# Performance work log

Measured on AMD Instinct MI355X. Metric: run time of the kernel, lower is better.

The kernel has to match this reference:

```python
import jax, jax.numpy as jnp
import numpy as np

DIM = 768; DEPTH = 8; HEADS = 12; DH = 64; DFF = 2048
SOFTCLAMP = 50.0; TIME_EVERY = 4
B, T, S = 2, 32, 256
EPS = 1e-6


def rmsnorm(x, w):
    return x * jax.lax.rsqrt(jnp.mean(x * x, axis=-1, keepdims=True) + EPS) * w


def l2norm(x):
    n = jnp.sqrt(jnp.sum(x * x, axis=-1, keepdims=True))
    return x / jnp.maximum(n, 1e-12)


def make_rotary(n):
    inv = 1.0 / (10000.0 ** (jnp.arange(0, DH, 2, dtype=jnp.float32) / DH))
    f = jnp.arange(n, dtype=jnp.float32)[:, None] * inv[None, :]
    return jnp.concatenate([f, f], axis=-1)  # (n, DH)


def apply_rot(rot, x):
    # x: (B', H, n, DH), rot: (n, DH)
    x1, x2 = jnp.split(x, 2, axis=-1)
    return x * jnp.cos(rot) + jnp.concatenate([-x2, x1], axis=-1) * jnp.sin(rot)


def attn_block(x, rv, nw, wq, wk, wv, wo, wg, wmix, bm, kgam, rot, causal):
    # x: (B', n, DIM); rv: (B', H, n, DH) value-residual
    Bp, n, _ = x.shape
    tn = rmsnorm(x, nw)
    q = (tn @ wq).reshape(Bp, n, HEADS, DH).transpose(0, 2, 1, 3)
    k = (tn @ wk).reshape(Bp, n, HEADS, DH).transpose(0, 2, 1, 3)
    v = (tn @ wv).reshape(Bp, n, HEADS, DH).transpose(0, 2, 1, 3)
    # learned value-residual lerp: v <- v + mix * (rv - v)
    mix = jax.nn.sigmoid(tn @ wmix + bm).transpose(0, 2, 1)[..., None]
    v = v + mix * (rv - v)
    # MultiHeadRMSNorm on keys: l2norm * (gamma+1) * sqrt(DH)
    k = l2norm(k) * ((kgam + 1.0) * (DH ** 0.5))[:, None, :]
    if rot is not None:
        q = apply_rot(rot, q)
        k = apply_rot(rot, k)
    sim = jnp.einsum('bhid,bhjd->bhij', q, k) * (DH ** -0.5)
    sim = jnp.tanh(sim / SOFTCLAMP) * SOFTCLAMP
    if causal:
        cm = jnp.triu(jnp.ones((n, n), dtype=bool), 1)
        sim = jnp.where(cm, -jnp.finfo(sim.dtype).max, sim)
    attn = jax.nn.softmax(sim, axis=-1)
    o = jnp.einsum('bhij,bhjd->bhid', attn, v)
    gates = jax.nn.sigmoid(tn @ wg).transpose(0, 2, 1)[..., None]
    o = o * gates
    o = o.transpose(0, 2, 1, 3).reshape(Bp, n, HEADS * DH)
    return o @ wo


def ff_block(x, nw, win, bi, wout, bo):
    tn = rmsnorm(x, nw)
    h = tn @ win + bi
    a, g = jnp.split(h, 2, axis=-1)
    return (a * jax.nn.gelu(g, approximate=False)) @ wout + bo


def setup_inputs() -> dict:
    key = jax.random.key(0)
    ks = jax.random.split(key, 16)
    def rn(k, shape, scale=0.02):
        return jax.random.normal(k, shape, dtype=jnp.float32) * scale
    return {
        'tokens': jax.random.normal(ks[0], (B, T, S, DIM), dtype=jnp.float32),
        'attn_norm_w': jnp.ones((DEPTH, DIM), jnp.float32),
        'Wq': rn(ks[1], (DEPTH, DIM, HEADS * DH)),
        'Wk': rn(ks[2], (DEPTH, DIM, HEADS * DH)),
        'Wv': rn(ks[3], (DEPTH, DIM, HEADS * DH)),
        'Wo': rn(ks[4], (DEPTH, HEADS * DH, DIM)),
        'Wg': rn(ks[5], (DEPTH, DIM, HEADS)),
        'Wmix': rn(ks[6], (DEPTH, DIM, HEADS)),
        'bmix': jnp.zeros((DEPTH, HEADS), jnp.float32),
        'k_gamma': rn(ks[7], (DEPTH, HEADS, DH)),
        'ff_norm_w': jnp.ones((DEPTH, DIM), jnp.float32),
        'Win': rn(ks[8], (DEPTH, DIM, 2 * DFF)),
        'b_in': jnp.zeros((DEPTH, 2 * DFF), jnp.float32),
        'Wout': rn(ks[9], (DEPTH, DFF, DIM)),
        'b_out': jnp.zeros((DEPTH, DIM), jnp.float32),
        'vr_norm_w': jnp.ones((DIM,), jnp.float32),
        'vr_W': rn(ks[10], (DIM, HEADS * DH)),
        'final_norm_w': jnp.ones((DIM,), jnp.float32),
    }


def reference(tokens, attn_norm_w, Wq, Wk, Wv, Wo, Wg, Wmix, bmix, k_gamma,
              ff_norm_w, Win, b_in, Wout, b_out, vr_norm_w, vr_W, final_norm_w):
    b, t, s, d = tokens.shape
    # value residuals computed once from the input tokens
    rv = (rmsnorm(tokens, vr_norm_w) @ vr_W).reshape(b, t, s, HEADS, DH)
    rot = make_rotary(t)
    x = tokens
    for i in range(DEPTH):
        is_time = ((i + 1) % TIME_EVERY == 0)
        if is_time:
            xa = x.transpose(0, 2, 1, 3).reshape(b * s, t, d)
            rva = rv.transpose(0, 2, 3, 1, 4).reshape(b * s, HEADS, t, DH)
            o = attn_block(xa, rva, attn_norm_w[i], Wq[i], Wk[i], Wv[i], Wo[i],
                           Wg[i], Wmix[i], bmix[i], k_gamma[i], rot, True)
            o = o.reshape(b, s, t, d).transpose(0, 2, 1, 3)
        else:
            xa = x.reshape(b * t, s, d)
            rva = rv.transpose(0, 1, 3, 2, 4).reshape(b * t, HEADS, s, DH)
            o = attn_block(xa, rva, attn_norm_w[i], Wq[i], Wk[i], Wv[i], Wo[i],
                           Wg[i], Wmix[i], bmix[i], k_gamma[i], None, False)
            o = o.reshape(b, t, s, d)
        x = x + o
        x = x + ff_block(x, ff_norm_w[i], Win[i], b_in[i], Wout[i], b_out[i])
    return rmsnorm(x, final_norm_w)
```

## Files before the change

kernel.cpp:

```cpp
#include <hip/hip_runtime.h>
#include <cmath>

#define DIM 768
#define DEPTH 8
#define HEADS 12
#define DH 64
#define DFF 2048
#define NTOK 16384
#define BB 2
#define TT 32
#define SS 256
#define LDQ 2304

typedef __attribute__((ext_vector_type(8))) short short8;
typedef __attribute__((ext_vector_type(4))) float f32x4;

__device__ __forceinline__ float sigmoidf_(float x) { return 1.0f / (1.0f + __expf(-x)); }
__device__ __forceinline__ float geluf_(float x) {
  float z = fabsf(x) * 0.70710678118654752f;
  float t = __builtin_amdgcn_rcpf(fmaf(0.3275911f, z, 1.0f));
  float poly = t * fmaf(t, fmaf(t, fmaf(t, fmaf(t, 1.061405429f, -1.453152027f),
                    1.421413741f), -0.284496736f), 0.254829592f);
  float erfv = 1.0f - poly * __expf(-z * z);
  erfv = copysignf(erfv, x);
  return 0.5f * x * (1.0f + erfv);
}
__device__ __forceinline__ unsigned short f2bf(float x) {
  union { float f; unsigned int u; } a; a.f = x;
  unsigned int r = a.u + 0x7fff + ((a.u >> 16) & 1);
  return (unsigned short)(r >> 16);
}
__device__ __forceinline__ float bf2f(unsigned short h) {
  union { unsigned int u; float f; } a; a.u = ((unsigned int)h) << 16;
  return a.f;
}
__device__ __forceinline__ void load_lds16(const void* g, void* l) {
  __builtin_amdgcn_global_load_lds(
      (const __attribute__((address_space(1))) unsigned int*)g,
      (__attribute__((address_space(3))) unsigned int*)l, 16, 0, 0);
}
__device__ __forceinline__ float softclamp_exp(float sv) {
  float a = exp2f(sv * 0.057707802f);
  float rc = __builtin_amdgcn_rcpf(a + 1.0f);
  return exp2f(fmaf(-144.26950408f, rc, 72.13475204f));
}

template<int BF>
__global__ __launch_bounds__(256) void rmsnorm_kernel(
    const float* __restrict__ x, const float* __restrict__ w, void* __restrict__ outp)
{
  int row = blockIdx.x;
  int tid = threadIdx.x;
  const float* xr = x + (size_t)row * DIM;
  float v0 = xr[tid], v1 = xr[tid + 256], v2 = xr[tid + 512];
  float ss = v0 * v0 + v1 * v1 + v2 * v2;
  #pragma unroll
  for (int off = 32; off; off >>= 1) ss += __shfl_xor(ss, off);
  __shared__ float sred[4];
  if ((tid & 63) == 0) sred[tid >> 6] = ss;
  __syncthreads();
  float tot = sred[0] + sred[1] + sred[2] + sred[3];
  float r = rsqrtf(tot * (1.0f / DIM) + 1e-6f);
  if (BF) {
    unsigned short* orow = (unsigned short*)outp + (size_t)row * DIM;
    orow[tid]       = f2bf(v0 * r * w[tid]);
    orow[tid + 256] = f2bf(v1 * r * w[tid + 256]);
    orow[tid + 512] = f2bf(v2 * r * w[tid + 512]);
  } else {
    float* orow = (float*)outp + (size_t)row * DIM;
    orow[tid]       = v0 * r * w[tid];
    orow[tid + 256] = v1 * r * w[tid + 256];
    orow[tid + 512] = v2 * r * w[tid + 512];
  }
}

__global__ __launch_bounds__(256) void w_to_bt(
    const float* __restrict__ W, unsigned short* __restrict__ WT, int K, int N)
{
  __shared__ float t[32][33];
  int n0 = blockIdx.x * 32, k0 = blockIdx.y * 32;
  int c = threadIdx.x & 31, r8 = threadIdx.x >> 5;
  #pragma unroll
  for (int rr = r8; rr < 32; rr += 8)
    t[rr][c] = W[(size_t)(k0 + rr) * N + n0 + c];
  __syncthreads();
  #pragma unroll
  for (int rn = r8; rn < 32; rn += 8)
    WT[(size_t)(n0 + rn) * K + k0 + c] = f2bf(t[c][rn]);
}

__global__ __launch_bounds__(256) void w_convert_layer(
    const float* __restrict__ Wq, const float* __restrict__ Wk,
    const float* __restrict__ Wv, const float* __restrict__ Wo,
    const float* __restrict__ Win, const float* __restrict__ Wout,
    unsigned short* __restrict__ wqkvT, unsigned short* __restrict__ woT,
    unsigned short* __restrict__ winT, unsigned short* __restrict__ woutT)
{
  __shared__ float tle[32][33];
  int t = blockIdx.x;
  const float* W; unsigned short* WT; int K, N, n0, k0, glu = 0;
  if (t < 1728) {
    int rg = t / 576, tt = t - rg * 576;
    W = (rg == 0) ? Wq : (rg == 1) ? Wk : Wv;
    WT = wqkvT + (size_t)rg * 768 * 768;
    K = 768; N = 768; n0 = (tt % 24) * 32; k0 = (tt / 24) * 32;
  } else if (t < 2304) {
    int tt = t - 1728; W = Wo; WT = woT;
    K = 768; N = 768; n0 = (tt % 24) * 32; k0 = (tt / 24) * 32;
  } else if (t < 5376) {
    int tt = t - 2304; W = Win; WT = winT;
    K = 768; N = 4096; n0 = (tt % 128) * 32; k0 = (tt / 128) * 32; glu = 1;
  } else {
    int tt = t - 5376; W = Wout; WT = woutT;
    K = 2048; N = 768; n0 = (tt % 24) * 32; k0 = (tt / 24) * 32;
  }
  int c = threadIdx.x & 31, r8 = threadIdx.x >> 5;
  int col = n0 + c;
  int scol = col;
  if (glu) {
    int b = col >> 5, rr2 = col & 31;
    scol = (rr2 < 16) ? (b * 16 + rr2) : (2048 + b * 16 + rr2 - 16);
  }
  for (int rr = r8; rr < 32; rr += 8)
    tle[rr][c] = W[(size_t)(k0 + rr) * N + scol];
  __syncthreads();
  for (int rn = r8; rn < 32; rn += 8)
    WT[(size_t)(n0 + rn) * K + k0 + c] = f2bf(tle[c][rn]);
}

template<int MODE>
__global__ __launch_bounds__(256) void gemm_bf16(
    const unsigned short* __restrict__ A, const unsigned short* __restrict__ BT,
    float* __restrict__ Cf, unsigned short* __restrict__ Hg,
    const float* __restrict__ bias, int M, int N, int K)
{
  __shared__ unsigned short As[128 * 64];
  __shared__ unsigned short Bs[128 * 64];
  const int tid = threadIdx.x;
  const int wave = tid >> 6;
  const int lane = tid & 63;
  const int bm = blockIdx.y * 128;
  const int bn = blockIdx.x * 128;
  const int wm = (wave & 1) * 64;
  const int wn = (wave >> 1) * 64;

  f32x4 acc[4][4];
  #pragma unroll
  for (int i = 0; i < 4; ++i)
    #pragma unroll
    for (int j = 0; j < 4; ++j) acc[i][j] = (f32x4){0.f, 0.f, 0.f, 0.f};

  const int srow = wave * 8 + (lane >> 3);
  const int sku = ((lane & 7) ^ (lane >> 3)) * 8;
  const unsigned short* gA = A + (size_t)(bm + srow) * K + sku;
  const unsigned short* gB = BT + (size_t)(bn + srow) * K + sku;
  unsigned short* lA = &As[wave * 512];
  unsigned short* lB = &Bs[wave * 512];

  const int fr = lane & 15;
  const int fg = lane >> 4;

  for (int k0 = 0; k0 < K; k0 += 64) {
    #pragma unroll
    for (int it = 0; it < 4; ++it) {
      load_lds16(gA + k0 + (size_t)(it * 32) * K, lA + it * 2048);
      load_lds16(gB + k0 + (size_t)(it * 32) * K, lB + it * 2048);
    }
    __syncthreads();
    #pragma unroll
    for (int s = 0; s < 2; ++s) {
      short8 a[4], b[4];
      #pragma unroll
      for (int i = 0; i < 4; ++i) {
        int row = wm + 16 * i + fr;
        a[i] = *(const short8*)&As[row * 64 + (((s * 4 + fg) ^ (row & 7)) << 3)];
      }
      #pragma unroll
      for (int j = 0; j < 4; ++j) {
        int row = wn + 16 * j + fr;
        b[j] = *(const short8*)&Bs[row * 64 + (((s * 4 + fg) ^ (row & 7)) << 3)];
      }
      #pragma unroll
      for (int i = 0; i < 4; ++i)
        #pragma unroll
        for (int j = 0; j < 4; ++j)
          acc[i][j] = __builtin_amdgcn_mfma_f32_16x16x32_bf16(a[i], b[j], acc[i][j], 0, 0, 0);
    }
    __syncthreads();
  }

  const int crow0 = bm + wm + (lane >> 4) * 4;
  const int ccol0 = bn + wn + fr;
  float bv[4];
  if (MODE != 3) {
    #pragma unroll
    for (int j = 0; j < 4; ++j) bv[j] = bias ? bias[ccol0 + 16 * j] : 0.0f;
  }
  #pragma unroll
  for (int i = 0; i < 4; ++i) {
    #pragma unroll
    for (int r = 0; r < 4; ++r) {
      int row = crow0 + 16 * i + r;
      if (MODE == 3) {
        #pragma unroll
        for (int pj = 0; pj < 2; ++pj) {
          int b32 = (bn + wn + 32 * pj) >> 5;
          float av = acc[i][2 * pj][r] + bias[b32 * 16 + fr];
          float gv = acc[i][2 * pj + 1][r] + bias[2048 + b32 * 16 + fr];
          Hg[(size_t)row * (N >> 1) + b32 * 16 + fr] = f2bf(av * geluf_(gv));
        }
      } else {
        #pragma unroll
        for (int j = 0; j < 4; ++j) {
          int col = ccol0 + 16 * j;
          size_t idx = (size_t)row * N + col;
          float val = acc[i][j][r] + bv[j];
          if (MODE == 0) Cf[idx] = val;
          else if (MODE == 1) Cf[idx] += val;
          else Hg[idx] = f2bf(val);
        }
      }
    }
  }
}

__global__ __launch_bounds__(256) void proj12x2_kernel(
    const unsigned short* __restrict__ A, const float* __restrict__ Bw1,
    const float* __restrict__ b1, const float* __restrict__ Bw2,
    float* __restrict__ out1, float* __restrict__ out2)
{
  int row = blockIdx.x * 4 + (threadIdx.x >> 6);
  int lane = threadIdx.x & 63;
  const unsigned short* ar = A + (size_t)row * DIM;
  float acc1[HEADS], acc2[HEADS];
  #pragma unroll
  for (int j = 0; j < HEADS; ++j) { acc1[j] = 0.0f; acc2[j] = 0.0f; }
  for (int k2 = lane; k2 < DIM; k2 += 64) {
    float a = bf2f(ar[k2]);
    const float* bw1 = Bw1 + (size_t)k2 * HEADS;
    const float* bw2 = Bw2 + (size_t)k2 * HEADS;
    #pragma unroll
    for (int j = 0; j < HEADS; ++j) {
      acc1[j] = fmaf(a, bw1[j], acc1[j]);
      acc2[j] = fmaf(a, bw2[j], acc2[j]);
    }
  }
  #pragma unroll
  for (int j = 0; j < HEADS; ++j) {
    #pragma unroll
    for (int off = 32; off; off >>= 1) {
      acc1[j] += __shfl_xor(acc1[j], off);
      acc2[j] += __shfl_xor(acc2[j], off);
    }
  }
  if (lane < HEADS) {
    out1[(size_t)row * HEADS + lane] = sigmoidf_(acc1[lane] + b1[lane]);
    out2[(size_t)row * HEADS + lane] = sigmoidf_(acc2[lane]);
  }
}

__global__ __launch_bounds__(768) void qkv_fix_kernel(
    unsigned short* __restrict__ qkv, const unsigned short* __restrict__ rvb,
    const float* __restrict__ mix, const float* __restrict__ kgam, int is_time)
{
  int tok = blockIdx.x;
  int h = threadIdx.x >> 6;
  int d = threadIdx.x & 63;
  size_t rowb = (size_t)tok * LDQ + h * DH + d;
  float kv = bf2f(qkv[rowb + 768]);
  float ss = kv * kv;
  #pragma unroll
  for (int off = 32; off; off >>= 1) ss += __shfl_xor(ss, off);
  float nrm = fmaxf(sqrtf(ss), 1e-12f);
  kv = kv / nrm * (kgam[h * DH + d] + 1.0f) * 8.0f;
  float mv = mix[(size_t)tok * HEADS + h];
  float vv = bf2f(qkv[rowb + 1536]);
  float rvv = bf2f(rvb[(size_t)tok * DIM + h * DH + d]);
  qkv[rowb + 1536] = f2bf(vv + mv * (rvv - vv));
  float qv = bf2f(qkv[rowb]);
  if (is_time) {
    int t = (tok >> 8) & 31;
    int j = d & 31;
    float ang = (float)t * __expf(-(float)j * (9.210340371976184f / 32.0f));
    float cs = cosf(ang), sn = sinf(ang);
    float qp = __shfl_xor(qv, 32);
    float kp = __shfl_xor(kv, 32);
    float sgn = (d < 32) ? -1.0f : 1.0f;
    qv = qv * cs + sgn * qp * sn;
    kv = kv * cs + sgn * kp * sn;
  }
  qkv[rowb] = f2bf(qv);
  qkv[rowb + 768] = f2bf(kv);
}

__global__ __launch_bounds__(256, 2) void attn_mfma_kernel(
    const unsigned short* __restrict__ q, const unsigned short* __restrict__ k,
    const unsigned short* __restrict__ v, const unsigned short* __restrict__ rvb,
    const float* __restrict__ mix, const float* __restrict__ gate,
    const float* __restrict__ kgam, unsigned short* __restrict__ o)
{
  __shared__ __align__(16) unsigned short Ks[128 * 64];
  __shared__ __align__(16) unsigned short VsT[64 * 128];
  __shared__ __align__(16) unsigned short Pw[4][32 * 64];
  const int tid = threadIdx.x;
  const int wave = tid >> 6;
  const int lane = tid & 63;
  const int g = lane >> 4;
  const int c16 = lane & 15;
  const int bp = blockIdx.x >> 1;
  const int qh = blockIdx.x & 1;
  const int h = blockIdx.y;
  const size_t qoff = (size_t)bp * SS * LDQ + h * DH;
  const int qbase = qh * 128 + wave * 32;

  short8 aq[2][2];
  #pragma unroll
  for (int i = 0; i < 2; ++i) {
    const unsigned short* qp = q + qoff + (size_t)(qbase + i * 16 + c16) * LDQ;
    #pragma unroll
    for (int cc = 0; cc < 2; ++cc)
      aq[i][cc] = *(const short8*)(qp + cc * 32 + g * 8);
  }

  f32x4 oacc[2][4];
  float rs[2][4];
  #pragma unroll
  for (int i = 0; i < 2; ++i)
    #pragma unroll
    for (int j = 0; j < 4; ++j) {
      oacc[i][j] = (f32x4){0.f, 0.f, 0.f, 0.f};
      rs[i][j] = 0.f;
    }

  for (int half = 0; half < 2; ++half) {
    const int r0 = half * 128;
    #pragma unroll
    for (int it = 0; it < 4; ++it) {
      int f = tid + it * 256;
      int row = f >> 3, u = f & 7;
      short8 t8 = *(const short8*)(k + qoff + (size_t)(r0 + row) * LDQ + u * 8);
      float kv[8];
      float ss = 0.f;
      #pragma unroll
      for (int c = 0; c < 8; ++c) { kv[c] = bf2f((unsigned short)t8[c]); ss += kv[c] * kv[c]; }
      ss += __shfl_xor(ss, 1); ss += __shfl_xor(ss, 2); ss += __shfl_xor(ss, 4);
      float inv = 8.0f / fmaxf(sqrtf(ss), 1e-12f);
      float4 kg0 = *(const float4*)(kgam + h * DH + u * 8);
      float4 kg1 = *(const float4*)(kgam + h * DH + u * 8 + 4);
      short8 o8;
      o8[0] = (short)f2bf(kv[0] * inv * (kg0.x + 1.0f));
      o8[1] = (short)f2bf(kv[1] * inv * (kg0.y + 1.0f));
      o8[2] = (short)f2bf(kv[2] * inv * (kg0.z + 1.0f));
      o8[3] = (short)f2bf(kv[3] * inv * (kg0.w + 1.0f));
      o8[4] = (short)f2bf(kv[4] * inv * (kg1.x + 1.0f));
      o8[5] = (short)f2bf(kv[5] * inv * (kg1.y + 1.0f));
      o8[6] = (short)f2bf(kv[6] * inv * (kg1.z + 1.0f));
      o8[7] = (short)f2bf(kv[7] * inv * (kg1.w + 1.0f));
      *(short8*)&Ks[row * 64 + ((u ^ (row & 7)) << 3)] = o8;
    }
    #pragma unroll
    for (int it = 0; it < 4; ++it) {
      int f = tid + it * 256;
      int j = f & 127, dq = f >> 7;
      int tok = bp * SS + r0 + j;
      short8 v8 = *(const short8*)(v + qoff + (size_t)(r0 + j) * LDQ + dq * 8);
      short8 r8 = *(const short8*)(rvb + (size_t)tok * DIM + h * DH + dq * 8);
      float mv = mix[(size_t)tok * HEADS + h];
      int u = j >> 3;
      #pragma unroll
      for (int c = 0; c < 8; ++c) {
        int d = dq * 8 + c;
        float vv = bf2f((unsigned short)v8[c]);
        float val = vv + mv * (bf2f((unsigned short)r8[c]) - vv);
        VsT[d * 128 + ((u ^ (d & 15)) << 3) + (j & 7)] = f2bf(val);
      }
    }
    __syncthreads();

    #pragma unroll
    for (int jc = 0; jc < 2; ++jc) {
      const int lr0 = jc * 64;
      #pragma unroll
      for (int jh = 0; jh < 2; ++jh) {
        f32x4 s[2][2];
        #pragma unroll
        for (int i = 0; i < 2; ++i)
          #pragma unroll
          for (int j = 0; j < 2; ++j) s[i][j] = (f32x4){0.f, 0.f, 0.f, 0.f};
        #pragma unroll
        for (int j2 = 0; j2 < 2; ++j2) {
          int jt = jh * 2 + j2;
          int row = lr0 + jt * 16 + c16;
          short8 b0 = *(const short8*)&Ks[row * 64 + ((g ^ (row & 7)) << 3)];
          short8 b1 = *(const short8*)&Ks[row * 64 + (((4 + g) ^ (row & 7)) << 3)];
          #pragma unroll
          for (int i = 0; i < 2; ++i) {
            s[i][j2] = __builtin_amdgcn_mfma_f32_16x16x32_bf16(aq[i][0], b0, s[i][j2], 0, 0, 0);
            s[i][j2] = __builtin_amdgcn_mfma_f32_16x16x32_bf16(aq[i][1], b1, s[i][j2], 0, 0, 0);
          }
        }
        #pragma unroll
        for (int i = 0; i < 2; ++i) {
          #pragma unroll
          for (int j2 = 0; j2 < 2; ++j2) {
            int pj = (jh * 2 + j2) * 16 + c16;
            int uj = pj >> 3;
            #pragma unroll
            for (int r = 0; r < 4; ++r) {
              float p = softclamp_exp(s[i][j2][r] * 0.125f);
              unsigned short pb = f2bf(p);
              rs[i][r] += bf2f(pb);
              int prow = i * 16 + g * 4 + r;
              Pw[wave][prow * 64 + ((uj ^ (prow & 7)) << 3) + (pj & 7)] = pb;
            }
          }
        }
      }
      #pragma unroll
      for (int jj = 0; jj < 2; ++jj) {
        short8 pa[2];
        #pragma unroll
        for (int i = 0; i < 2; ++i) {
          int prow = i * 16 + c16;
          int u = jj * 4 + g;
          pa[i] = *(const short8*)&Pw[wave][prow * 64 + ((u ^ (prow & 7)) << 3)];
        }
        const int jl = lr0 + jj * 32 + g * 8;
        const int uv = jl >> 3;
        #pragma unroll
        for (int dt = 0; dt < 4; ++dt) {
          int d = dt * 16 + c16;
          short8 bv = *(const short8*)&VsT[d * 128 + ((uv ^ (d & 15)) << 3)];
          #pragma unroll
          for (int i = 0; i < 2; ++i)
            oacc[i][dt] = __builtin_amdgcn_mfma_f32_16x16x32_bf16(pa[i], bv, oacc[i][dt], 0, 0, 0);
        }
      }
    }
    __syncthreads();
  }

  #pragma unroll
  for (int i = 0; i < 2; ++i)
    #pragma unroll
    for (int r = 0; r < 4; ++r) {
      float t = rs[i][r];
      t += __shfl_xor(t, 1); t += __shfl_xor(t, 2);
      t += __shfl_xor(t, 4); t += __shfl_xor(t, 8);
      rs[i][r] = t;
    }
  #pragma unroll
  for (int i = 0; i < 2; ++i) {
    #pragma unroll
    for (int r = 0; r < 4; ++r) {
      int row = qbase + i * 16 + g * 4 + r;
      int tq = bp * SS + row;
      float gt = gate[(size_t)tq * HEADS + h] / rs[i][r];
      unsigned short* op = o + (size_t)tq * DIM + h * DH;
      #pragma unroll
      for (int dt = 0; dt < 4; ++dt)
        op[dt * 16 + c16] = f2bf(oacc[i][dt][r] * gt);
    }
  }
}

__global__ __launch_bounds__(256, 2) void attn_time_mfma(
    const unsigned short* __restrict__ q, const unsigned short* __restrict__ k,
    const unsigned short* __restrict__ v, const float* __restrict__ gate,
    unsigned short* __restrict__ o)
{
  __shared__ __align__(16) unsigned short VT[4][64 * 32];
  __shared__ __align__(16) unsigned short Pw[4][32 * 32];
  const int tid = threadIdx.x;
  const int wave = tid >> 6;
  const int lane = tid & 63;
  const int g = lane >> 4;
  const int c16 = lane & 15;
  const int h = blockIdx.y;
  const int sp = blockIdx.x * 4 + wave;
  const int base = (sp >> 8) * (TT * SS) + (sp & 255);

  short8 aq[2][2], bk[2][2];
  #pragma unroll
  for (int i = 0; i < 2; ++i) {
    const unsigned short* qp = q + (size_t)(base + (i * 16 + c16) * SS) * LDQ + h * DH;
    const unsigned short* kp = k + (size_t)(base + (i * 16 + c16) * SS) * LDQ + h * DH;
    #pragma unroll
    for (int cc = 0; cc < 2; ++cc) {
      aq[i][cc] = *(const short8*)(qp + cc * 32 + g * 8);
      bk[i][cc] = *(const short8*)(kp + cc * 32 + g * 8);
    }
  }

  {
    int tp = lane >> 1;
    int dh0 = (lane & 1) * 32;
    const unsigned short* vp = v + (size_t)(base + tp * SS) * LDQ + h * DH + dh0;
    int ut = tp >> 3;
    #pragma unroll
    for (int j4 = 0; j4 < 4; ++j4) {
      short8 t = *(const short8*)(vp + j4 * 8);
      #pragma unroll
      for (int c = 0; c < 8; ++c) {
        int d = dh0 + j4 * 8 + c;
        VT[wave][d * 32 + ((ut ^ (d & 3)) << 3) + (tp & 7)] = (unsigned short)t[c];
      }
    }
  }

  f32x4 s[2][2];
  #pragma unroll
  for (int i = 0; i < 2; ++i)
    #pragma unroll
    for (int j = 0; j < 2; ++j) s[i][j] = (f32x4){0.f, 0.f, 0.f, 0.f};
  #pragma unroll
  for (int jt = 0; jt < 2; ++jt)
    #pragma unroll
    for (int i = 0; i < 2; ++i) {
      s[i][jt] = __builtin_amdgcn_mfma_f32_16x16x32_bf16(aq[i][0], bk[jt][0], s[i][jt], 0, 0, 0);
      s[i][jt] = __builtin_amdgcn_mfma_f32_16x16x32_bf16(aq[i][1], bk[jt][1], s[i][jt], 0, 0, 0);
    }

  float rs[2][4];
  #pragma unroll
  for (int i = 0; i < 2; ++i)
    #pragma unroll
    for (int r = 0; r < 4; ++r) rs[i][r] = 0.f;
  #pragma unroll
  for (int i = 0; i < 2; ++i) {
    #pragma unroll
    for (int jt = 0; jt < 2; ++jt) {
      int pj = jt * 16 + c16;
      int uj = pj >> 3;
      #pragma unroll
      for (int r = 0; r < 4; ++r) {
        int t = i * 16 + g * 4 + r;
        float p = softclamp_exp(s[i][jt][r] * 0.125f);
        unsigned short pb = (pj <= t) ? f2bf(p) : (unsigned short)0;
        rs[i][r] += bf2f(pb);
        Pw[wave][t * 32 + ((uj ^ (t & 3)) << 3) + (pj & 7)] = pb;
      }
    }
  }

  short8 pa[2];
  #pragma unroll
  for (int i = 0; i < 2; ++i) {
    int prow = i * 16 + c16;
    pa[i] = *(const short8*)&Pw[wave][prow * 32 + ((g ^ (prow & 3)) << 3)];
  }
  f32x4 oacc[2][4];
  #pragma unroll
  for (int dt = 0; dt < 4; ++dt) {
    int d = dt * 16 + c16;
    short8 bv = *(const short8*)&VT[wave][d * 32 + ((g ^ (d & 3)) << 3)];
    #pragma unroll
    for (int i = 0; i < 2; ++i)
      oacc[i][dt] = __builtin_amdgcn_mfma_f32_16x16x32_bf16(
          pa[i], bv, (f32x4){0.f, 0.f, 0.f, 0.f}, 0, 0, 0);
  }

  #pragma unroll
  for (int i = 0; i < 2; ++i)
    #pragma unroll
    for (int r = 0; r < 4; ++r) {
      float t = rs[i][r];
      t += __shfl_xor(t, 1); t += __shfl_xor(t, 2);
      t += __shfl_xor(t, 4); t += __shfl_xor(t, 8);
      rs[i][r] = t;
    }
  #pragma unroll
  for (int i = 0; i < 2; ++i) {
    #pragma unroll
    for (int r = 0; r < 4; ++r) {
      int t = i * 16 + g * 4 + r;
      int tok = base + t * SS;
      float gt = gate[(size_t)tok * HEADS + h] / rs[i][r];
      unsigned short* op = o + (size_t)tok * DIM + h * DH;
      #pragma unroll
      for (int dt = 0; dt < 4; ++dt)
        op[dt * 16 + c16] = f2bf(oacc[i][dt][r] * gt);
    }
  }
}

extern "C" void kernel_launch(void* const* d_in, const int* in_sizes, int n_in,
                              void* d_out, int out_size, void* d_ws, size_t ws_size,
                              hipStream_t stream)
{
  const float* tokens = (const float*)d_in[0];
  const float* attn_norm_w = (const float*)d_in[1];
  const float* Wq   = (const float*)d_in[2];
  const float* Wk   = (const float*)d_in[3];
  const float* Wv   = (const float*)d_in[4];
  const float* Wo   = (const float*)d_in[5];
  const float* Wg   = (const float*)d_in[6];
  const float* Wmix = (const float*)d_in[7];
  const float* bmix = (const float*)d_in[8];
  const float* kgam = (const float*)d_in[9];
  const float* ffw  = (const float*)d_in[10];
  const float* Win  = (const float*)d_in[11];
  const float* bin  = (const float*)d_in[12];
  const float* Wout = (const float*)d_in[13];
  const float* bout = (const float*)d_in[14];
  const float* vrw  = (const float*)d_in[15];
  const float* vrW  = (const float*)d_in[16];
  const float* fnw  = (const float*)d_in[17];

  const size_t NT = (size_t)NTOK * DIM;
  float* ws  = (float*)d_ws;
  float* x   = ws;
  float* mix = x + NT;
  float* gate = mix + (size_t)NTOK * HEADS;
  unsigned short* tn   = (unsigned short*)(gate + (size_t)NTOK * HEADS);
  unsigned short* qkv  = tn + NT;
  unsigned short* rvb  = qkv + (size_t)NTOK * LDQ;
  unsigned short* wqkvT = rvb + NT;
  unsigned short* woT  = wqkvT + (size_t)2304 * 768;
  unsigned short* winT = woT + (size_t)768 * 768;
  unsigned short* woutT= winT + (size_t)4096 * 768;
  unsigned short* vrWT = woutT + (size_t)768 * 2048;
  unsigned short* hg   = qkv;

  hipMemcpyAsync(x, tokens, NT * sizeof(float), hipMemcpyDeviceToDevice, stream);

  w_to_bt<<<dim3(24, 24), 256, 0, stream>>>(vrW, vrWT, DIM, DIM);
  rmsnorm_kernel<1><<<NTOK, 256, 0, stream>>>(tokens, vrw, tn);
  gemm_bf16<2><<<dim3(6, 128), 256, 0, stream>>>(
      tn, vrWT, nullptr, rvb, nullptr, NTOK, DIM, DIM);

  for (int i = 0; i < DEPTH; ++i) {
    int is_time = ((i + 1) % 4 == 0) ? 1 : 0;
    w_convert_layer<<<6912, 256, 0, stream>>>(
        Wq + (size_t)i * DIM * DIM, Wk + (size_t)i * DIM * DIM,
        Wv + (size_t)i * DIM * DIM, Wo + (size_t)i * DIM * DIM,
        Win + (size_t)i * DIM * 2 * DFF, Wout + (size_t)i * DFF * DIM,
        wqkvT, woT, winT, woutT);

    rmsnorm_kernel<1><<<NTOK, 256, 0, stream>>>(x, attn_norm_w + (size_t)i * DIM, tn);
    gemm_bf16<2><<<dim3(18, 128), 256, 0, stream>>>(
        tn, wqkvT, nullptr, qkv, nullptr, NTOK, LDQ, DIM);
    proj12x2_kernel<<<NTOK / 4, 256, 0, stream>>>(
        tn, Wmix + (size_t)i * DIM * HEADS, bmix + (size_t)i * HEADS,
        Wg + (size_t)i * DIM * HEADS, mix, gate);
    if (is_time) {
      qkv_fix_kernel<<<dim3(NTOK), 768, 0, stream>>>(
          qkv, rvb, mix, kgam + (size_t)i * HEADS * DH, is_time);
      attn_time_mfma<<<dim3((BB * SS) / 4, HEADS), 256, 0, stream>>>(
          qkv, qkv + 768, qkv + 1536, gate, tn);
    } else {
      attn_mfma_kernel<<<dim3(BB * TT * 2, HEADS), 256, 0, stream>>>(
          qkv, qkv + 768, qkv + 1536, rvb, mix, gate,
          kgam + (size_t)i * HEADS * DH, tn);
    }
    gemm_bf16<1><<<dim3(6, 128), 256, 0, stream>>>(tn, woT, x, nullptr, nullptr, NTOK, DIM, DIM);
    rmsnorm_kernel<1><<<NTOK, 256, 0, stream>>>(x, ffw + (size_t)i * DIM, tn);
    gemm_bf16<3><<<dim3(32, 128), 256, 0, stream>>>(
        tn, winT, nullptr, hg, bin + (size_t)i * 2 * DFF, NTOK, 2 * DFF, DIM);
    gemm_bf16<1><<<dim3(6, 128), 256, 0, stream>>>(
        hg, woutT, x, nullptr, bout + (size_t)i * DIM, NTOK, DIM, DFF);
  }
  rmsnorm_kernel<0><<<NTOK, 256, 0, stream>>>(x, fnw, (float*)d_out);
}
```

Measured before the change: 4.429 ms.

## Rewrite bf16 GEMM as 256x256 tile with double-buffered LDS ping-pong pipeline

```diff
diff --git a/kernel.cpp b/kernel.cpp
--- a/kernel.cpp
+++ b/kernel.cpp
@@ -129,67 +129,122 @@
 }
 
 template<int MODE>
-__global__ __launch_bounds__(256) void gemm_bf16(
+__global__ __launch_bounds__(512, 2) void gemm_bf16(
     const unsigned short* __restrict__ A, const unsigned short* __restrict__ BT,
     float* __restrict__ Cf, unsigned short* __restrict__ Hg,
     const float* __restrict__ bias, int M, int N, int K)
 {
-  __shared__ unsigned short As[128 * 64];
-  __shared__ unsigned short Bs[128 * 64];
+  __shared__ unsigned short As[2][256 * 64];
+  __shared__ unsigned short Bs[2][256 * 64];
   const int tid = threadIdx.x;
   const int wave = tid >> 6;
   const int lane = tid & 63;
-  const int bm = blockIdx.y * 128;
-  const int bn = blockIdx.x * 128;
-  const int wm = (wave & 1) * 64;
-  const int wn = (wave >> 1) * 64;
-
-  f32x4 acc[4][4];
-  #pragma unroll
-  for (int i = 0; i < 4; ++i)
-    #pragma unroll
-    for (int j = 0; j < 4; ++j) acc[i][j] = (f32x4){0.f, 0.f, 0.f, 0.f};
-
-  const int srow = wave * 8 + (lane >> 3);
-  const int sku = ((lane & 7) ^ (lane >> 3)) * 8;
-  const unsigned short* gA = A + (size_t)(bm + srow) * K + sku;
-  const unsigned short* gB = BT + (size_t)(bn + srow) * K + sku;
-  unsigned short* lA = &As[wave * 512];
-  unsigned short* lB = &Bs[wave * 512];
-
+  const int bm = blockIdx.y * 256;
+  const int bn = blockIdx.x * 256;
+  const int wm = (wave >> 2) * 128;
+  const int wn = (wave & 3) * 64;
   const int fr = lane & 15;
   const int fg = lane >> 4;
 
-  for (int k0 = 0; k0 < K; k0 += 64) {
-    #pragma unroll
-    for (int it = 0; it < 4; ++it) {
-      load_lds16(gA + k0 + (size_t)(it * 32) * K, lA + it * 2048);
-      load_lds16(gB + k0 + (size_t)(it * 32) * K, lB + it * 2048);
-    }
-    __syncthreads();
-    #pragma unroll
-    for (int s = 0; s < 2; ++s) {
-      short8 a[4], b[4];
-      #pragma unroll
-      for (int i = 0; i < 4; ++i) {
-        int row = wm + 16 * i + fr;
-        a[i] = *(const short8*)&As[row * 64 + (((s * 4 + fg) ^ (row & 7)) << 3)];
-      }
-      #pragma unroll
-      for (int j = 0; j < 4; ++j) {
-        int row = wn + 16 * j + fr;
-        b[j] = *(const short8*)&Bs[row * 64 + (((s * 4 + fg) ^ (row & 7)) << 3)];
-      }
-      #pragma unroll
-      for (int i = 0; i < 4; ++i)
-        #pragma unroll
-        for (int j = 0; j < 4; ++j)
-          acc[i][j] = __builtin_amdgcn_mfma_f32_16x16x32_bf16(a[i], b[j], acc[i][j], 0, 0, 0);
-    }
-    __syncthreads();
-  }
-
-  const int crow0 = bm + wm + (lane >> 4) * 4;
+  f32x4 acc[8][4];
+  #pragma unroll
+  for (int i = 0; i < 8; ++i)
+    #pragma unroll
+    for (int j = 0; j < 4; ++j) acc[i][j] = (f32x4){0.f, 0.f, 0.f, 0.f};
+
+  const unsigned short* gA0 = A + (size_t)(bm + wave * 8 + (lane >> 3)) * K
+                                + (((lane & 7) ^ (lane >> 3)) << 3);
+  const unsigned short* gB0 = BT + (size_t)(bn + wave * 8 + (lane >> 3)) * K
+                                 + (((lane & 7) ^ (lane >> 3)) << 3);
+
+#define STAGE_A(KT_, H_) { \
+  load_lds16(gA0 + (size_t)(128 * (H_)) * K + (KT_) * 64, \
+             &As[(KT_) & 1][(128 * (H_) + wave * 8) * 64]); \
+  load_lds16(gA0 + (size_t)(128 * (H_) + 64) * K + (KT_) * 64, \
+             &As[(KT_) & 1][(128 * (H_) + 64 + wave * 8) * 64]); }
+#define STAGE_B(KT_, H_) { \
+  load_lds16(gB0 + (size_t)(128 * (H_)) * K + (KT_) * 64, \
+             &Bs[(KT_) & 1][(128 * (H_) + wave * 8) * 64]); \
+  load_lds16(gB0 + (size_t)(128 * (H_) + 64) * K + (KT_) * 64, \
+             &Bs[(KT_) & 1][(128 * (H_) + 64 + wave * 8) * 64]); }
+
+  short8 a[4][2], b[2][2];
+
+#define LDA_HALF(IB, SL) { \
+  _Pragma("unroll") for (int ii = 0; ii < 4; ++ii) { \
+    int row_ = wm + 16 * ((IB) + ii) + fr; \
+    int rx_ = (row_ & 7) << 3; \
+    a[ii][0] = *(const short8*)&As[SL][row_ * 64 + ((fg << 3) ^ rx_)]; \
+    a[ii][1] = *(const short8*)&As[SL][row_ * 64 + ((32 + (fg << 3)) ^ rx_)]; } }
+#define LDB_PAIR(JB, SL) { \
+  _Pragma("unroll") for (int jj = 0; jj < 2; ++jj) { \
+    int row_ = wn + 16 * ((JB) + jj) + fr; \
+    int rx_ = (row_ & 7) << 3; \
+    b[jj][0] = *(const short8*)&Bs[SL][row_ * 64 + ((fg << 3) ^ rx_)]; \
+    b[jj][1] = *(const short8*)&Bs[SL][row_ * 64 + ((32 + (fg << 3)) ^ rx_)]; } }
+#define MFMA_Q(IB, JB) { \
+  _Pragma("unroll") for (int ii = 0; ii < 4; ++ii) \
+  _Pragma("unroll") for (int jj = 0; jj < 2; ++jj) { \
+    acc[(IB)+ii][(JB)+jj] = __builtin_amdgcn_mfma_f32_16x16x32_bf16( \
+        a[ii][0], b[jj][0], acc[(IB)+ii][(JB)+jj], 0, 0, 0); \
+    acc[(IB)+ii][(JB)+jj] = __builtin_amdgcn_mfma_f32_16x16x32_bf16( \
+        a[ii][1], b[jj][1], acc[(IB)+ii][(JB)+jj], 0, 0, 0); } }
+#define PH_MID() \
+  __builtin_amdgcn_s_barrier(); \
+  asm volatile("s_waitcnt lgkmcnt(0)" ::: "memory"); \
+  __builtin_amdgcn_sched_barrier(0); \
+  __builtin_amdgcn_s_setprio(1);
+#define PH_END() \
+  __builtin_amdgcn_s_setprio(0); \
+  __builtin_amdgcn_s_barrier();
+
+  const int KT = K >> 6;
+  const int ITERS = KT >> 1;
+
+  STAGE_A(0, 0); STAGE_A(0, 1); STAGE_B(0, 0); STAGE_B(0, 1); STAGE_A(1, 0);
+  asm volatile("s_waitcnt vmcnt(2)" ::: "memory");
+  __builtin_amdgcn_s_barrier();
+
+  for (int it = 0; it < ITERS; ++it) {
+    const int c1 = 2 * it + 1;
+    const int n0 = 2 * it + 2;
+    const bool last = (it == ITERS - 1);
+    LDA_HALF(0, 0); LDB_PAIR(0, 0);
+    STAGE_A(c1, 1);
+    PH_MID(); MFMA_Q(0, 0); PH_END();
+    LDB_PAIR(2, 0);
+    STAGE_B(c1, 0);
+    PH_MID(); MFMA_Q(0, 2); PH_END();
+    LDA_HALF(4, 0); LDB_PAIR(0, 0);
+    STAGE_B(c1, 1);
+    PH_MID(); MFMA_Q(4, 0); PH_END();
+    LDB_PAIR(2, 0);
+    if (n0 < KT) STAGE_A(n0, 0);
+    PH_MID(); MFMA_Q(4, 2);
+    __builtin_amdgcn_s_setprio(0);
+    if (!last) asm volatile("s_waitcnt vmcnt(2)" ::: "memory");
+    else       asm volatile("s_waitcnt vmcnt(0)" ::: "memory");
+    __builtin_amdgcn_s_barrier();
+    LDA_HALF(0, 1); LDB_PAIR(0, 1);
+    if (n0 < KT) STAGE_A(n0, 1);
+    PH_MID(); MFMA_Q(0, 0); PH_END();
+    LDB_PAIR(2, 1);
+    if (n0 < KT) STAGE_B(n0, 0);
+    PH_MID(); MFMA_Q(0, 2); PH_END();
+    LDA_HALF(4, 1); LDB_PAIR(0, 1);
+    if (n0 < KT) STAGE_B(n0, 1);
+    PH_MID(); MFMA_Q(4, 0); PH_END();
+    LDB_PAIR(2, 1);
+    if (c1 + 2 < KT) STAGE_A(c1 + 2, 0);
+    PH_MID(); MFMA_Q(4, 2);
+    __builtin_amdgcn_s_setprio(0);
+    if (!last) {
+      asm volatile("s_waitcnt vmcnt(2)" ::: "memory");
+      __builtin_amdgcn_s_barrier();
+    }
+  }
+
+  const int crow0 = bm + wm + ((lane >> 4) << 2);
   const int ccol0 = bn + wn + fr;
   float bv[4];
   if (MODE != 3) {
@@ -197,7 +252,7 @@
     for (int j = 0; j < 4; ++j) bv[j] = bias ? bias[ccol0 + 16 * j] : 0.0f;
   }
   #pragma unroll
-  for (int i = 0; i < 4; ++i) {
+  for (int i = 0; i < 8; ++i) {
     #pragma unroll
     for (int r = 0; r < 4; ++r) {
       int row = crow0 + 16 * i + r;
@@ -222,6 +277,13 @@
       }
     }
   }
+#undef STAGE_A
+#undef STAGE_B
+#undef LDA_HALF
+#undef LDB_PAIR
+#undef MFMA_Q
+#undef PH_MID
+#undef PH_END
 }
 
 __global__ __launch_bounds__(256) void proj12x2_kernel(
@@ -626,7 +688,7 @@
 
   w_to_bt<<<dim3(24, 24), 256, 0, stream>>>(vrW, vrWT, DIM, DIM);
   rmsnorm_kernel<1><<<NTOK, 256, 0, stream>>>(tokens, vrw, tn);
-  gemm_bf16<2><<<dim3(6, 128), 256, 0, stream>>>(
+  gemm_bf16<2><<<dim3(3, 64), 512, 0, stream>>>(
       tn, vrWT, nullptr, rvb, nullptr, NTOK, DIM, DIM);
 
   for (int i = 0; i < DEPTH; ++i) {
@@ -638,7 +700,7 @@
         wqkvT, woT, winT, woutT);
 
     rmsnorm_kernel<1><<<NTOK, 256, 0, stream>>>(x, attn_norm_w + (size_t)i * DIM, tn);
-    gemm_bf16<2><<<dim3(18, 128), 256, 0, stream>>>(
+    gemm_bf16<2><<<dim3(9, 64), 512, 0, stream>>>(
         tn, wqkvT, nullptr, qkv, nullptr, NTOK, LDQ, DIM);
     proj12x2_kernel<<<NTOK / 4, 256, 0, stream>>>(
         tn, Wmix + (size_t)i * DIM * HEADS, bmix + (size_t)i * HEADS,
@@ -653,11 +715,11 @@
           qkv, qkv + 768, qkv + 1536, rvb, mix, gate,
           kgam + (size_t)i * HEADS * DH, tn);
     }
-    gemm_bf16<1><<<dim3(6, 128), 256, 0, stream>>>(tn, woT, x, nullptr, nullptr, NTOK, DIM, DIM);
+    gemm_bf16<1><<<dim3(3, 64), 512, 0, stream>>>(tn, woT, x, nullptr, nullptr, NTOK, DIM, DIM);
     rmsnorm_kernel<1><<<NTOK, 256, 0, stream>>>(x, ffw + (size_t)i * DIM, tn);
-    gemm_bf16<3><<<dim3(32, 128), 256, 0, stream>>>(
+    gemm_bf16<3><<<dim3(16, 64), 512, 0, stream>>>(
         tn, winT, nullptr, hg, bin + (size_t)i * 2 * DFF, NTOK, 2 * DFF, DIM);
-    gemm_bf16<1><<<dim3(6, 128), 256, 0, stream>>>(
+    gemm_bf16<1><<<dim3(3, 64), 512, 0, stream>>>(
         hg, woutT, x, nullptr, bout + (size_t)i * DIM, NTOK, DIM, DFF);
   }
   rmsnorm_kernel<0><<<NTOK, 256, 0, stream>>>(x, fnw, (float*)d_out);
```

Measured after the change: 4.368 ms. Within noise of the previous version (-1.4%).
